# Optimization experiments

Hardware: AMD Instinct MI355X
Metric: run time of the kernel (lower is better)

The kernel has to match this reference:

```python
import jax, jax.numpy as jnp
import numpy as np

N_HEADS = 8

def setup_inputs() -> dict:
    key = jax.random.key(0)
    ks = jax.random.split(key, 5)
    C = 256
    x = jax.random.normal(ks[0], (4, C, 48, 48), dtype=jnp.float32)
    w_qkv = jax.random.normal(ks[1], (3 * C, C), dtype=jnp.float32) * (C ** -0.5)
    b_qkv = jax.random.normal(ks[2], (3 * C,), dtype=jnp.float32) * 0.02
    w_proj = jax.random.normal(ks[3], (C, C), dtype=jnp.float32) * (C ** -0.5)
    b_proj = jax.random.normal(ks[4], (C,), dtype=jnp.float32) * 0.02
    return {"x": x, "w_qkv": w_qkv, "b_qkv": b_qkv, "w_proj": w_proj, "b_proj": b_proj}


def reference(x, w_qkv, b_qkv, w_proj, b_proj):
    B, C, H, W = x.shape
    h = N_HEADS
    dh = C // h
    N = H * W
    # flatten spatial dims to tokens: [B, N, C]
    xf = x.reshape(B, C, N).transpose(0, 2, 1)
    # fused qkv projection (torch Linear: y = x @ W.T + b)
    qkv = xf @ w_qkv.T + b_qkv                      # [B, N, 3C]
    qkv = qkv.reshape(B, N, 3, h, dh).transpose(2, 0, 3, 1, 4)  # [3, B, h, N, dh]
    q, k, v = qkv[0], qkv[1], qkv[2]
    scale = dh ** -0.5
    attn = jax.nn.softmax(jnp.einsum('bhnd,bhmd->bhnm', q, k) * scale, axis=-1)
    out = jnp.einsum('bhnm,bhmd->bhnd', attn, v)    # [B, h, N, dh]
    out = out.transpose(0, 2, 1, 3).reshape(B, N, C)
    out = out @ w_proj.T + b_proj                   # [B, N, C]
    return out.transpose(0, 2, 1).reshape(B, C, H, W)
```

## Files before the change

### kernel.cpp

```cpp
#include <hip/hip_runtime.h>
#include <hip/hip_bf16.h>

#define B_    4
#define C_    256
#define NTOK  2304
#define NH    8
#define DH    32

typedef short bf16x8 __attribute__((ext_vector_type(8)));
typedef short bf16x4 __attribute__((ext_vector_type(4)));
typedef float f32x4  __attribute__((ext_vector_type(4)));

__device__ __forceinline__ short rne_bf16(float f) {
    union { float f; unsigned u; } v; v.f = f;
    const unsigned r = v.u + 0x7fffu + ((v.u >> 16) & 1u);
    return (short)(r >> 16);
}
__device__ __forceinline__ unsigned pack2_bf16(float a, float b) {
    return (unsigned)(unsigned short)rne_bf16(a) | ((unsigned)(unsigned short)rne_bf16(b) << 16);
}
__device__ __forceinline__ float fast_exp2(float x) {
#if __has_builtin(__builtin_amdgcn_exp2f)
    return __builtin_amdgcn_exp2f(x);
#else
    return exp2f(x);
#endif
}

__global__ __launch_bounds__(256) void prep_kernel(
    const float* __restrict__ wq, const float* __restrict__ wp,
    short* __restrict__ wqb, short* __restrict__ wpb)
{
    const int id = blockIdx.x * 256 + threadIdx.x;
    const int base = id * 16;
    #pragma unroll
    for (int u = 0; u < 4; ++u) {
        const int off = base + u * 4;
        float4 v; short* d;
        if (off < 196608) { v = *(const float4*)(wq + off); d = wqb + off; }
        else { v = *(const float4*)(wp + (off - 196608)); d = wpb + (off - 196608); }
        d[0] = rne_bf16(v.x); d[1] = rne_bf16(v.y);
        d[2] = rne_bf16(v.z); d[3] = rne_bf16(v.w);
    }
}

__global__ __launch_bounds__(256) void qkv_mfma(
    const float* __restrict__ x,
    const short* __restrict__ wqb,
    const float* __restrict__ bias,
    short* __restrict__ qb, short* __restrict__ kb, short* __restrict__ vt)
{
    __shared__ short As[32][264];
    __shared__ short Es[4][2560];
    const int t    = threadIdx.x;
    const int wave = t >> 6;
    const int lane = t & 63;
    const int quad = lane >> 4, l16 = lane & 15;
    const int blk  = blockIdx.x;
    const int b    = blk / 216;
    const int rem  = blk % 216;
    const int mt   = rem / 3;
    const int jg   = rem % 3;
    const int m0   = mt * 32;
    const int j0   = (jg * 4 + wave) * 64;

    {
        const int n4  = (t & 7) * 4;
        const int tc2 = t >> 3;
        const float* xb = x + ((size_t)b * C_) * NTOK + m0 + n4;
        #pragma unroll
        for (int r = 0; r < 4; ++r) {
            const int c = tc2 * 2 + r * 64;
            const float4 v0 = *(const float4*)(xb + (size_t)c * NTOK);
            const float4 v1 = *(const float4*)(xb + (size_t)(c + 1) * NTOK);
            *(unsigned*)&As[n4 + 0][c] = pack2_bf16(v0.x, v1.x);
            *(unsigned*)&As[n4 + 1][c] = pack2_bf16(v0.y, v1.y);
            *(unsigned*)&As[n4 + 2][c] = pack2_bf16(v0.z, v1.z);
            *(unsigned*)&As[n4 + 3][c] = pack2_bf16(v0.w, v1.w);
        }
    }
    __syncthreads();

    const short* bbase = wqb + (size_t)(j0 + l16) * C_ + quad * 8;

    f32x4 acc[2][4] = {};
    for (int k0 = 0; k0 < C_; k0 += 32) {
        bf16x8 af[2], bfr[4];
        #pragma unroll
        for (int i = 0; i < 2; ++i)
            af[i] = *(const bf16x8*)&As[i * 16 + l16][k0 + quad * 8];
        #pragma unroll
        for (int j = 0; j < 4; ++j)
            bfr[j] = *(const bf16x8*)(bbase + (size_t)j * 16 * C_ + k0);
        #pragma unroll
        for (int i = 0; i < 2; ++i)
            #pragma unroll
            for (int j = 0; j < 4; ++j)
                acc[i][j] = __builtin_amdgcn_mfma_f32_16x16x32_bf16(af[i], bfr[j], acc[i][j], 0, 0, 0);
    }

    short* Ew = Es[wave];
    const int three = j0 >> 8;
    if (three < 2) {
        const float sc = (three == 0) ? 0.25503486f : 1.0f;
        #pragma unroll
        for (int j = 0; j < 4; ++j) {
            const float bv = bias[j0 + j * 16 + l16];
            #pragma unroll
            for (int i = 0; i < 2; ++i)
                #pragma unroll
                for (int r = 0; r < 4; ++r) {
                    const int n_l = i * 16 + quad * 4 + r;
                    Ew[n_l * 72 + j * 16 + l16] = rne_bf16((acc[i][j][r] + bv) * sc);
                }
        }
        const int n_l = lane & 31, hh = lane >> 5;
        const int head = ((j0 + hh * 32) >> 5) & 7;
        short* dst = ((three == 0) ? qb : kb)
                   + ((size_t)(b * NH + head) * NTOK + m0 + n_l) * DH;
        #pragma unroll
        for (int s = 0; s < 4; ++s)
            *(bf16x8*)(dst + s * 8) = *(const bf16x8*)&Ew[n_l * 72 + hh * 32 + s * 8];
    } else {
        #pragma unroll
        for (int j = 0; j < 4; ++j) {
            const float bv = bias[j0 + j * 16 + l16];
            const int j_l = j * 16 + l16;
            #pragma unroll
            for (int i = 0; i < 2; ++i) {
                const int nb = i * 16 + quad * 4;
                *(unsigned*)&Ew[j_l * 40 + nb] =
                    pack2_bf16(acc[i][j][0] + bv, acc[i][j][1] + bv);
                *(unsigned*)&Ew[j_l * 40 + nb + 2] =
                    pack2_bf16(acc[i][j][2] + bv, acc[i][j][3] + bv);
            }
        }
        #pragma unroll
        for (int p = 0; p < 4; ++p) {
            const int j_r = p * 16 + (lane >> 2);
            const int seg = (lane & 3) * 8;
            const int head = ((j0 + j_r) >> 5) & 7;
            const int d    = j_r & 31;
            *(bf16x8*)(vt + ((size_t)(b * NH + head) * DH + d) * NTOK + m0 + seg) =
                *(const bf16x8*)&Ew[j_r * 40 + seg];
        }
    }
}

__global__ __launch_bounds__(256) void attn_kernel(
    const short* __restrict__ qg,
    const short* __restrict__ kg,
    const short* __restrict__ vg,
    float* __restrict__ po,
    float* __restrict__ pl)
{
    const int bh   = blockIdx.y;
    const int q0   = blockIdx.x * 64;
    const int half = blockIdx.z;
    const int t    = threadIdx.x;
    const int wave = t >> 6;
    const int lane = t & 63;
    const int quad = lane >> 4;
    const int l16  = lane & 15;

    __shared__ short Ks[64][40];
    __shared__ short Vt[32][72];
    __shared__ short Ps[4][16][68];

    const short* kbase = kg + (size_t)bh * NTOK * DH;
    const short* vbase = vg + (size_t)bh * DH * NTOK;

    const short* qptr = qg + ((size_t)bh * NTOK + q0 + wave * 16 + l16) * DH + quad * 8;
    const bf16x8 qf = *(const bf16x8*)qptr;

    f32x4 Oc0 = {0.f, 0.f, 0.f, 0.f};
    f32x4 Oc1 = {0.f, 0.f, 0.f, 0.f};
    float lpart[4] = {0.f, 0.f, 0.f, 0.f};

    const int kbeg = half * (NTOK / 2);
    const int kend = kbeg + (NTOK / 2);

    const int kr = t >> 2, ksg = t & 3;
    const int vr = t >> 3, vsg = t & 7;

    bf16x8 kreg = *(const bf16x8*)(kbase + (size_t)(kbeg + kr) * DH + ksg * 8);
    bf16x8 vreg = *(const bf16x8*)(vbase + (size_t)vr * NTOK + kbeg + vsg * 8);

    for (int kt = kbeg; kt < kend; kt += 64) {
        *(bf16x8*)&Ks[kr][ksg * 8] = kreg;
        *(bf16x8*)&Vt[vr][vsg * 8] = vreg;
        __syncthreads();

        const int ktn = (kt + 64 < kend) ? kt + 64 : kbeg;
        kreg = *(const bf16x8*)(kbase + (size_t)(ktn + kr) * DH + ksg * 8);
        vreg = *(const bf16x8*)(vbase + (size_t)vr * NTOK + ktn + vsg * 8);

        f32x4 S[4];
        #pragma unroll
        for (int jt = 0; jt < 4; ++jt) {
            const bf16x8 kf = *(const bf16x8*)&Ks[jt * 16 + l16][quad * 8];
            f32x4 z = {0.f, 0.f, 0.f, 0.f};
            S[jt] = __builtin_amdgcn_mfma_f32_16x16x32_bf16(qf, kf, z, 0, 0, 0);
        }

        #pragma unroll
        for (int jt = 0; jt < 4; ++jt) {
            #pragma unroll
            for (int r = 0; r < 4; ++r) {
                const float p = fast_exp2(S[jt][r]);
                lpart[r] += p;
                Ps[wave][quad * 4 + r][jt * 16 + l16] = rne_bf16(p);
            }
        }

        #pragma unroll
        for (int jc = 0; jc < 2; ++jc) {
            const bf16x4 p0 = *(const bf16x4*)&Ps[wave][l16][jc * 32 + quad * 8];
            const bf16x4 p1 = *(const bf16x4*)&Ps[wave][l16][jc * 32 + quad * 8 + 4];
            bf16x8 af;
            af[0] = p0[0]; af[1] = p0[1]; af[2] = p0[2]; af[3] = p0[3];
            af[4] = p1[0]; af[5] = p1[1]; af[6] = p1[2]; af[7] = p1[3];
            const bf16x8 b0 = *(const bf16x8*)&Vt[l16][jc * 32 + quad * 8];
            const bf16x8 b1 = *(const bf16x8*)&Vt[16 + l16][jc * 32 + quad * 8];
            Oc0 = __builtin_amdgcn_mfma_f32_16x16x32_bf16(af, b0, Oc0, 0, 0, 0);
            Oc1 = __builtin_amdgcn_mfma_f32_16x16x32_bf16(af, b1, Oc1, 0, 0, 0);
        }
        __syncthreads();
    }

    #pragma unroll
    for (int off = 1; off < 16; off <<= 1) {
        #pragma unroll
        for (int r = 0; r < 4; ++r)
            lpart[r] += __shfl_xor(lpart[r], off, 64);
    }

    const size_t rowbase = ((size_t)half * 32 + bh) * NTOK + q0 + wave * 16 + quad * 4;
    float* obase = po + rowbase * DH + l16;
    #pragma unroll
    for (int r = 0; r < 4; ++r) {
        obase[(size_t)r * DH]      = Oc0[r];
        obase[(size_t)r * DH + 16] = Oc1[r];
    }
    if (l16 == 0) {
        float* lb = pl + rowbase;
        #pragma unroll
        for (int r = 0; r < 4; ++r) lb[r] = lpart[r];
    }
}

__global__ __launch_bounds__(256) void proj_mfma(
    const float* __restrict__ po,
    const float* __restrict__ pl,
    const short* __restrict__ wpb,
    const float* __restrict__ bias,
    float* __restrict__ out)
{
    __shared__ short Ac[32 * 336];
    __shared__ float Ep[4][2304];
    const int t    = threadIdx.x;
    const int wave = t >> 6;
    const int lane = t & 63;
    const int quad = lane >> 4, l16 = lane & 15;
    const int blk  = blockIdx.x;
    const int b    = blk / 72;
    const int mt   = blk % 72;
    const int m0   = mt * 32;
    const int c0   = wave * 64;

    const size_t PO_OFF = (size_t)32 * NTOK * DH;
    const size_t PL_OFF = (size_t)32 * NTOK;

    {
        const int m  = t >> 3;
        const int d4 = (t & 7) * 4;
        #pragma unroll
        for (int h = 0; h < NH; ++h) {
            const size_t row  = (size_t)(b * NH + h) * NTOK + m0 + m;
            const float inv = 1.f / (pl[row] + pl[PL_OFF + row]);
            const float* p0 = po + row * DH + d4;
            const f32x4 a = *(const f32x4*)p0;
            const f32x4 c = *(const f32x4*)(p0 + PO_OFF);
            short* dst = &Ac[m * 336 + h * 40 + d4];
            *(unsigned*)dst       = pack2_bf16((a[0] + c[0]) * inv, (a[1] + c[1]) * inv);
            *(unsigned*)(dst + 2) = pack2_bf16((a[2] + c[2]) * inv, (a[3] + c[3]) * inv);
        }
    }
    __syncthreads();

    const short* bbase = wpb + (size_t)(c0 + l16) * C_ + quad * 8;

    f32x4 acc[2][4] = {};
    for (int kt = 0; kt < 8; ++kt) {
        bf16x8 af[2], bfr[4];
        #pragma unroll
        for (int i = 0; i < 2; ++i)
            af[i] = *(const bf16x8*)&Ac[(i * 16 + l16) * 336 + kt * 40 + quad * 8];
        #pragma unroll
        for (int j = 0; j < 4; ++j)
            bfr[j] = *(const bf16x8*)(bbase + (size_t)j * 16 * C_ + kt * 32);
        #pragma unroll
        for (int i = 0; i < 2; ++i)
            #pragma unroll
            for (int j = 0; j < 4; ++j)
                acc[i][j] = __builtin_amdgcn_mfma_f32_16x16x32_bf16(af[i], bfr[j], acc[i][j], 0, 0, 0);
    }

    float* Ew = Ep[wave];
    #pragma unroll
    for (int j = 0; j < 4; ++j) {
        const int j_l = j * 16 + l16;
        const float bv = bias[c0 + j_l];
        #pragma unroll
        for (int i = 0; i < 2; ++i) {
            f32x4 st = {acc[i][j][0] + bv, acc[i][j][1] + bv,
                        acc[i][j][2] + bv, acc[i][j][3] + bv};
            *(f32x4*)&Ew[j_l * 36 + i * 16 + quad * 4] = st;
        }
    }
    #pragma unroll
    for (int p = 0; p < 8; ++p) {
        const int c_r = p * 8 + (lane >> 3);
        const int seg = (lane & 7) * 4;
        *(float4*)(out + ((size_t)b * C_ + c0 + c_r) * NTOK + m0 + seg) =
            *(const float4*)&Ew[c_r * 36 + seg];
    }
}

extern "C" void kernel_launch(void* const* d_in, const int* in_sizes, int n_in,
                              void* d_out, int out_size, void* d_ws, size_t ws_size,
                              hipStream_t stream) {
    const float* x      = (const float*)d_in[0];
    const float* w_qkv  = (const float*)d_in[1];
    const float* b_qkv  = (const float*)d_in[2];
    const float* w_proj = (const float*)d_in[3];
    const float* b_proj = (const float*)d_in[4];
    float* out = (float*)d_out;

    const size_t SZ = (size_t)B_ * NH * NTOK * DH;
    short* wqb = (short*)d_ws;
    short* wpb = wqb + 196608;
    short* qb  = wpb + 65536;
    short* kb  = qb + SZ;
    short* vt  = kb + SZ;
    float* po  = (float*)(vt + SZ);
    float* pl  = po + 2 * SZ;

    prep_kernel<<<64, 256, 0, stream>>>(w_qkv, w_proj, wqb, wpb);
    qkv_mfma<<<864, 256, 0, stream>>>(x, wqb, b_qkv, qb, kb, vt);
    attn_kernel<<<dim3(36, 32, 2), 256, 0, stream>>>(qb, kb, vt, po, pl);
    proj_mfma<<<288, 256, 0, stream>>>(po, pl, wpb, b_proj, out);
}
```

Baseline: 159.5 us.

## Load K/V fragments directly from global memory and use hardware bf16 pack conversion

The attention kernel stops staging K and V tiles through shared memory with block-wide barriers. Each wave now loads its MFMA K and V operand fragments straight from global memory, relying on L1/L2 to serve the reuse across waves. This removes both __syncthreads per iteration and the LDS round-trip, but drops the software prefetch, so each wave reads K/V from global redundantly and may stall on load latency. Separately, the bf16 rounding helpers switch to the packed hardware conversion builtin when available, and the weight-prep kernel writes packed 32-bit pairs.

```diff
diff --git a/kernel.cpp b/kernel.cpp
--- a/kernel.cpp
+++ b/kernel.cpp
@@ -11,6 +11,16 @@
 typedef short bf16x4 __attribute__((ext_vector_type(4)));
 typedef float f32x4  __attribute__((ext_vector_type(4)));
 
+#if __has_builtin(__builtin_amdgcn_cvt_pk_bf16_f32)
+__device__ __forceinline__ unsigned pack2_bf16(float a, float b) {
+    auto v = __builtin_amdgcn_cvt_pk_bf16_f32(a, b);
+    return __builtin_bit_cast(unsigned, v);
+}
+__device__ __forceinline__ short rne_bf16(float f) {
+    auto v = __builtin_amdgcn_cvt_pk_bf16_f32(f, f);
+    return (short)(__builtin_bit_cast(unsigned, v) & 0xffffu);
+}
+#else
 __device__ __forceinline__ short rne_bf16(float f) {
     union { float f; unsigned u; } v; v.f = f;
     const unsigned r = v.u + 0x7fffu + ((v.u >> 16) & 1u);
@@ -19,6 +29,7 @@
 __device__ __forceinline__ unsigned pack2_bf16(float a, float b) {
     return (unsigned)(unsigned short)rne_bf16(a) | ((unsigned)(unsigned short)rne_bf16(b) << 16);
 }
+#endif
 __device__ __forceinline__ float fast_exp2(float x) {
 #if __has_builtin(__builtin_amdgcn_exp2f)
     return __builtin_amdgcn_exp2f(x);
@@ -39,8 +50,8 @@
         float4 v; short* d;
         if (off < 196608) { v = *(const float4*)(wq + off); d = wqb + off; }
         else { v = *(const float4*)(wp + (off - 196608)); d = wpb + (off - 196608); }
-        d[0] = rne_bf16(v.x); d[1] = rne_bf16(v.y);
-        d[2] = rne_bf16(v.z); d[3] = rne_bf16(v.w);
+        *(unsigned*)d       = pack2_bf16(v.x, v.y);
+        *(unsigned*)(d + 2) = pack2_bf16(v.z, v.w);
     }
 }
 
@@ -163,8 +174,6 @@
     const int quad = lane >> 4;
     const int l16  = lane & 15;
 
-    __shared__ short Ks[64][40];
-    __shared__ short Vt[32][72];
     __shared__ short Ps[4][16][68];
 
     const short* kbase = kg + (size_t)bh * NTOK * DH;
@@ -172,35 +181,25 @@
 
     const short* qptr = qg + ((size_t)bh * NTOK + q0 + wave * 16 + l16) * DH + quad * 8;
     const bf16x8 qf = *(const bf16x8*)qptr;
+
+    const short* kfp = kbase + (size_t)(half * (NTOK / 2) + l16) * DH + quad * 8;
+    const short* vfp0 = vbase + (size_t)l16 * NTOK + half * (NTOK / 2) + quad * 8;
+    const short* vfp1 = vfp0 + (size_t)16 * NTOK;
 
     f32x4 Oc0 = {0.f, 0.f, 0.f, 0.f};
     f32x4 Oc1 = {0.f, 0.f, 0.f, 0.f};
     float lpart[4] = {0.f, 0.f, 0.f, 0.f};
 
-    const int kbeg = half * (NTOK / 2);
-    const int kend = kbeg + (NTOK / 2);
-
-    const int kr = t >> 2, ksg = t & 3;
-    const int vr = t >> 3, vsg = t & 7;
-
-    bf16x8 kreg = *(const bf16x8*)(kbase + (size_t)(kbeg + kr) * DH + ksg * 8);
-    bf16x8 vreg = *(const bf16x8*)(vbase + (size_t)vr * NTOK + kbeg + vsg * 8);
-
-    for (int kt = kbeg; kt < kend; kt += 64) {
-        *(bf16x8*)&Ks[kr][ksg * 8] = kreg;
-        *(bf16x8*)&Vt[vr][vsg * 8] = vreg;
-        __syncthreads();
-
-        const int ktn = (kt + 64 < kend) ? kt + 64 : kbeg;
-        kreg = *(const bf16x8*)(kbase + (size_t)(ktn + kr) * DH + ksg * 8);
-        vreg = *(const bf16x8*)(vbase + (size_t)vr * NTOK + ktn + vsg * 8);
-
+    for (int it = 0; it < (NTOK / 2) / 64; ++it) {
+        bf16x8 kf[4];
+        #pragma unroll
+        for (int jt = 0; jt < 4; ++jt)
+            kf[jt] = *(const bf16x8*)(kfp + (size_t)(it * 64 + jt * 16) * DH);
         f32x4 S[4];
         #pragma unroll
         for (int jt = 0; jt < 4; ++jt) {
-            const bf16x8 kf = *(const bf16x8*)&Ks[jt * 16 + l16][quad * 8];
             f32x4 z = {0.f, 0.f, 0.f, 0.f};
-            S[jt] = __builtin_amdgcn_mfma_f32_16x16x32_bf16(qf, kf, z, 0, 0, 0);
+            S[jt] = __builtin_amdgcn_mfma_f32_16x16x32_bf16(qf, kf[jt], z, 0, 0, 0);
         }
 
         #pragma unroll
@@ -220,12 +219,11 @@
             bf16x8 af;
             af[0] = p0[0]; af[1] = p0[1]; af[2] = p0[2]; af[3] = p0[3];
             af[4] = p1[0]; af[5] = p1[1]; af[6] = p1[2]; af[7] = p1[3];
-            const bf16x8 b0 = *(const bf16x8*)&Vt[l16][jc * 32 + quad * 8];
-            const bf16x8 b1 = *(const bf16x8*)&Vt[16 + l16][jc * 32 + quad * 8];
+            const bf16x8 b0 = *(const bf16x8*)(vfp0 + it * 64 + jc * 32);
+            const bf16x8 b1 = *(const bf16x8*)(vfp1 + it * 64 + jc * 32);
             Oc0 = __builtin_amdgcn_mfma_f32_16x16x32_bf16(af, b0, Oc0, 0, 0, 0);
             Oc1 = __builtin_amdgcn_mfma_f32_16x16x32_bf16(af, b1, Oc1, 0, 0, 0);
         }
-        __syncthreads();
     }
 
     #pragma unroll
```

After: 214.7 us. +34.6%, slower.
